# Kernel tuning notes

Measured on AMD Instinct MI355X. Metric: run time of the kernel, lower is better.

Reference implementation:

```python
import jax, jax.numpy as jnp
import numpy as np

K = 5  # kernel_size per dim, dim=2 -> 25 kernel weights, degree-1 open B-splines


def _spline_basis(pseudo):
    """Degree-1 open B-spline basis for dim=2, kernel_size=5.
    pseudo: [E,2] in [0,1]. Returns basis [E,4], kernel index wi [E,4]."""
    v = pseudo * (K - 1)                      # [E,2]
    lo = jnp.floor(v)
    frac = v - lo                             # [E,2]
    lo = lo.astype(jnp.int32)
    b = jnp.stack([1.0 - frac, frac], axis=-1)            # [E,2,2] (edge, dim, offset)
    idx = jnp.clip(lo[..., None] + jnp.arange(2, dtype=jnp.int32), 0, K - 1)  # [E,2,2]
    basis = b[:, 0, :, None] * b[:, 1, None, :]           # [E,2,2]
    wi = idx[:, 0, :, None] + K * idx[:, 1, None, :]      # [E,2,2] (dim0 stride 1, dim1 stride K)
    E = pseudo.shape[0]
    return basis.reshape(E, 4), wi.reshape(E, 4)


def _spline_conv(x, src, dst, pseudo, W, root, bias, num_nodes):
    basis, wi = _spline_basis(pseudo)          # [E,4], [E,4]
    xW = jnp.einsum('ni,kio->nko', x, W)       # [N,25,out]
    gathered = xW[src[:, None], wi]            # [E,4,out]
    msg = jnp.einsum('es,eso->eo', basis, gathered)  # [E,out]
    agg = jax.ops.segment_max(msg, dst, num_segments=num_nodes)
    agg = jnp.where(jnp.isneginf(agg), 0.0, agg)  # empty segments -> 0 (PyG fill)
    return agg + x @ root + bias


def setup_inputs() -> dict:
    key = jax.random.key(0)
    ks = jax.random.split(key, 12)
    N, E, C = 50000, 800000, 64
    s = 1.0 / np.sqrt(C)
    return {
        'x': jax.random.normal(ks[0], (N, C), jnp.float32),
        'edge_index': jax.random.randint(ks[1], (2, E), 0, N, jnp.int32),
        'edge_attr': jax.random.uniform(ks[2], (E, 2), jnp.float32),
        'W1': jax.random.normal(ks[3], (25, C, C), jnp.float32) * s,
        'root1': jax.random.normal(ks[4], (C, C), jnp.float32) * s,
        'b1': jnp.zeros((C,), jnp.float32),
        'W2': jax.random.normal(ks[5], (25, C, C), jnp.float32) * s,
        'root2': jax.random.normal(ks[6], (C, C), jnp.float32) * s,
        'b2': jnp.zeros((C,), jnp.float32),
        'final_w': jax.random.normal(ks[7], (3 * C, C), jnp.float32) / np.sqrt(3 * C),
        'final_b': jnp.zeros((C,), jnp.float32),
    }


def reference(x, edge_index, edge_attr, W1, root1, b1, W2, root2, b2, final_w, final_b):
    N = x.shape[0]
    src, dst = edge_index[0], edge_index[1]
    x1 = jax.nn.relu(_spline_conv(x, src, dst, edge_attr, W1, root1, b1, N))
    x2 = jax.nn.relu(_spline_conv(x1, src, dst, edge_attr, W2, root2, b2, N))
    h = jnp.concatenate([x, x1, x2], axis=-1)   # cat=True; dropout p=0 (eval)
    return h @ final_w + final_b
```

## Files before the change

kernel.cpp:

```cpp
#include <hip/hip_runtime.h>
#include <hip/hip_bf16.h>


typedef short  bf16x8 __attribute__((ext_vector_type(8)));
typedef float  f32x4  __attribute__((ext_vector_type(4)));

__device__ __forceinline__ float bf2f(ushort u) {
    return __uint_as_float((uint)u << 16);
}
__device__ __forceinline__ ushort f2bf(float f) {
    uint u = __float_as_uint(f);
    return (ushort)((u + 0x7FFF + ((u >> 16) & 1)) >> 16);
}

__global__ __launch_bounds__(256) void prep(
    const float* __restrict__ x, ushort* __restrict__ xb, int nx,
    const float* __restrict__ W1, const float* __restrict__ r1, ushort* __restrict__ WtA,
    const float* __restrict__ W2, const float* __restrict__ r2, ushort* __restrict__ WtB,
    const float* __restrict__ fw, ushort* __restrict__ fwT,
    int* __restrict__ deg, int N)
{
    const int nw = 26 * 4096, nfw = 3 * 4096;
    int idx = blockIdx.x * 256 + threadIdx.x;
    if (idx < nx) { xb[idx] = f2bf(x[idx]); return; }
    idx -= nx;
    if (idx < nw) {
        int tile = idx >> 12, rem = idx & 4095, o = rem >> 6, i = rem & 63;
        WtA[idx] = f2bf(tile < 25 ? W1[tile * 4096 + i * 64 + o] : r1[i * 64 + o]);
        return;
    }
    idx -= nw;
    if (idx < nw) {
        int tile = idx >> 12, rem = idx & 4095, o = rem >> 6, i = rem & 63;
        WtB[idx] = f2bf(tile < 25 ? W2[tile * 4096 + i * 64 + o] : r2[i * 64 + o]);
        return;
    }
    idx -= nw;
    if (idx < nfw) {
        int t = idx >> 12, rem = idx & 4095, o = rem >> 6, k = rem & 63;
        fwT[idx] = f2bf(fw[(t * 64 + k) * 64 + o]);
        return;
    }
    idx -= nfw;
    if (idx < N) deg[idx] = 0;
}

__global__ __launch_bounds__(256) void hist_deg(
    const int* __restrict__ ei, int* __restrict__ deg, int E)
{
    int e = blockIdx.x * 256 + threadIdx.x;
    if (e < E) atomicAdd(&deg[ei[E + e]], 1);
}

__global__ __launch_bounds__(1024) void scan_block(
    const int* __restrict__ deg, int* __restrict__ inc,
    int* __restrict__ partial, int N)
{
    __shared__ int s[1024];
    int i = blockIdx.x * 1024 + threadIdx.x;
    int v = (i < N) ? deg[i] : 0;
    s[threadIdx.x] = v;
    __syncthreads();
    for (int off = 1; off < 1024; off <<= 1) {
        int t = (threadIdx.x >= off) ? s[threadIdx.x - off] : 0;
        __syncthreads();
        s[threadIdx.x] += t;
        __syncthreads();
    }
    if (i < N) inc[i] = s[threadIdx.x];
    if (threadIdx.x == 1023) partial[blockIdx.x] = s[1023];
}

__global__ void scan_partial(int* __restrict__ partial, int nb)
{
    __shared__ int s[64];
    int t = threadIdx.x;
    int v = (t < nb) ? partial[t] : 0;
    s[t] = v;
    __syncthreads();
    for (int off = 1; off < 64; off <<= 1) {
        int x = (t >= off) ? s[t - off] : 0;
        __syncthreads();
        s[t] += x;
        __syncthreads();
    }
    if (t < nb) partial[t] = s[t] - v;
}

__global__ __launch_bounds__(1024) void scan_finalize(
    const int* __restrict__ deg, const int* __restrict__ inc,
    const int* __restrict__ partial, int* __restrict__ row_ptr,
    int* __restrict__ cursor, int N)
{
    int i = blockIdx.x * 1024 + threadIdx.x;
    if (i >= N) return;
    int v = inc[i] + partial[blockIdx.x];
    row_ptr[i + 1] = v;
    cursor[i] = v - deg[i];
    if (i == 0) row_ptr[0] = 0;
}

__global__ __launch_bounds__(256) void gemm_scatter(
    const ushort* __restrict__ A, const ushort* __restrict__ Wt,
    ushort* __restrict__ xWb, float* __restrict__ xRoot, int mtiles,
    const int* __restrict__ ei, const float* __restrict__ attr,
    int* __restrict__ cursor, int4* __restrict__ epack, int E)
{
    __shared__ ushort Cs[64][72];
    const int bx = blockIdx.x;

    if (bx >= 26) {
        if (!ei) return;
        int e = ((bx - 26) * gridDim.y + blockIdx.y) * 256 + threadIdx.x;
        if (e >= E) return;
        int src = ei[e], dst = ei[E + e];
        float u = attr[2 * e] * 4.f;
        float v = attr[2 * e + 1] * 4.f;
        float lu = floorf(u), lv = floorf(v);
        float fu = u - lu, fv = v - lv;
        int iu = (int)lu;  iu = iu < 0 ? 0 : (iu > 4 ? 4 : iu);
        int iv = (int)lv;  iv = iv < 0 ? 0 : (iv > 4 ? 4 : iv);
        int iu1 = iu + 1 > 4 ? 4 : iu + 1;
        int iv1 = iv + 1 > 4 ? 4 : iv + 1;
        uint slots = (uint)(iu + 5 * iv) | ((uint)(iu + 5 * iv1) << 8) |
                     ((uint)(iu1 + 5 * iv) << 16) | ((uint)(iu1 + 5 * iv1) << 24);
        uint wlo = (uint)f2bf((1.f - fu) * (1.f - fv)) | ((uint)f2bf((1.f - fu) * fv) << 16);
        uint whi = (uint)f2bf(fu * (1.f - fv)) | ((uint)f2bf(fu * fv) << 16);
        int pos = atomicAdd(&cursor[dst], 1);
        epack[pos] = make_int4(src * 3200, (int)slots, (int)wlo, (int)whi);
        return;
    }

    const int wave = threadIdx.x >> 6;
    const int lane = threadIdx.x & 63;
    const int l16 = lane & 15;
    const int half = lane >> 4;
    const int tid = threadIdx.x;

    const ushort* btile = Wt + (size_t)bx * 4096;
    bf16x8 b0[4], b1[4];
    #pragma unroll
    for (int s = 0; s < 4; ++s) {
        const ushort* brow = btile + (size_t)(s * 16 + l16) * 64;
        b0[s] = *(const bf16x8*)(brow + half * 8);
        b1[s] = *(const bf16x8*)(brow + 32 + half * 8);
    }

    for (int it = 0; it < 8; ++it) {
        const int mt = blockIdx.y * 8 + it;
        if (mt >= mtiles) break;
        const int m0 = mt * 64;
        const int m_base = m0 + wave * 16;

        const ushort* arow = A + (size_t)(m_base + l16) * 64;
        bf16x8 a0 = *(const bf16x8*)(arow + half * 8);
        bf16x8 a1 = *(const bf16x8*)(arow + 32 + half * 8);

        f32x4 acc[4];
        #pragma unroll
        for (int s = 0; s < 4; ++s) {
            acc[s] = (f32x4){0.f, 0.f, 0.f, 0.f};
            acc[s] = __builtin_amdgcn_mfma_f32_16x16x32_bf16(a0, b0[s], acc[s], 0, 0, 0);
            acc[s] = __builtin_amdgcn_mfma_f32_16x16x32_bf16(a1, b1[s], acc[s], 0, 0, 0);
        }

        if (bx == 25) {
            #pragma unroll
            for (int s = 0; s < 4; ++s)
                #pragma unroll
                for (int r = 0; r < 4; ++r)
                    xRoot[(size_t)(m_base + half * 4 + r) * 64 + s * 16 + l16] = acc[s][r];
            continue;
        }

        #pragma unroll
        for (int s = 0; s < 4; ++s)
            #pragma unroll
            for (int r = 0; r < 4; ++r)
                Cs[wave * 16 + half * 4 + r][s * 16 + l16] = f2bf(acc[s][r]);
        __syncthreads();
        #pragma unroll
        for (int i2 = 0; i2 < 2; ++i2) {
            int idx = tid + i2 * 256;
            int row = idx >> 3, seg = idx & 7;
            uint4 v = *(const uint4*)&Cs[row][seg * 8];
            *(uint4*)(xWb + (size_t)(m0 + row) * 1600 + bx * 64 + seg * 8) = v;
        }
        __syncthreads();
    }
}

__device__ __forceinline__ void gather4(
    const char* __restrict__ xwb, int lane, int rb, uint slots, ushort g[4])
{
    g[0] = *((const ushort*)(xwb + rb + ((slots & 255u) << 7)) + lane);
    g[1] = *((const ushort*)(xwb + rb + (((slots >> 8) & 255u) << 7)) + lane);
    g[2] = *((const ushort*)(xwb + rb + (((slots >> 16) & 255u) << 7)) + lane);
    g[3] = *((const ushort*)(xwb + rb + ((slots >> 24) << 7)) + lane);
}

__device__ __forceinline__ float consume4(const int4 d, const ushort g[4])
{
    float m = __uint_as_float((uint)d.z << 16) * bf2f(g[0]);
    m = fmaf(__uint_as_float((uint)d.z & 0xffff0000u), bf2f(g[1]), m);
    m = fmaf(__uint_as_float((uint)d.w << 16), bf2f(g[2]), m);
    m = fmaf(__uint_as_float((uint)d.w & 0xffff0000u), bf2f(g[3]), m);
    return m;
}

__global__ __launch_bounds__(256) void edge_csr(
    const ushort* __restrict__ xWb, const int* __restrict__ row_ptr,
    const int4* __restrict__ epack, const float* __restrict__ xRoot,
    const float* __restrict__ bias, float* __restrict__ outf,
    ushort* __restrict__ outb, int N)
{
    const int wv = __builtin_amdgcn_readfirstlane(threadIdx.x >> 6);
    const int d = blockIdx.x * 4 + wv;
    const int lane = threadIdx.x & 63;
    if (d >= N) return;
    const int e0 = __builtin_amdgcn_readfirstlane(row_ptr[d]);
    const int e1 = __builtin_amdgcn_readfirstlane(row_ptr[d + 1]);
    const char* xwb = (const char*)xWb;

    float vmax = -__builtin_inff();
    int e = e0;
    const int pairs = (e1 - e0) >> 1;
    if (pairs > 0) {
        int4 dA = epack[e], dB = epack[e + 1];
        ushort gA[4], gB[4];
        gather4(xwb, lane, dA.x, (uint)dA.y, gA);
        gather4(xwb, lane, dB.x, (uint)dB.y, gB);
        for (int p = 1; p < pairs; ++p) {
            int4 nA = epack[e + 2 * p], nB = epack[e + 2 * p + 1];
            ushort hA[4], hB[4];
            gather4(xwb, lane, nA.x, (uint)nA.y, hA);
            gather4(xwb, lane, nB.x, (uint)nB.y, hB);
            vmax = fmaxf(vmax, fmaxf(consume4(dA, gA), consume4(dB, gB)));
            #pragma unroll
            for (int i = 0; i < 4; ++i) { gA[i] = hA[i]; gB[i] = hB[i]; }
            dA = nA; dB = nB;
        }
        vmax = fmaxf(vmax, fmaxf(consume4(dA, gA), consume4(dB, gB)));
        e += pairs * 2;
    }
    if (e < e1) {
        int4 dA = epack[e];
        ushort gA[4];
        gather4(xwb, lane, dA.x, (uint)dA.y, gA);
        vmax = fmaxf(vmax, consume4(dA, gA));
    }
    if (e1 == e0) vmax = 0.f;
    float val = vmax + xRoot[(size_t)d * 64 + lane] + bias[lane];
    val = fmaxf(val, 0.f);
    if (outf) outf[(size_t)d * 64 + lane] = val;
    if (outb) outb[(size_t)d * 64 + lane] = f2bf(val);
}

__global__ __launch_bounds__(256) void final_mfma(
    const ushort* __restrict__ xb, const ushort* __restrict__ x1b,
    const ushort* __restrict__ x2b, const ushort* __restrict__ fwT,
    const float* __restrict__ fb, float* __restrict__ out, int M)
{
    const int wave = threadIdx.x >> 6;
    const int lane = threadIdx.x & 63;
    const int l16 = lane & 15;
    const int half = lane >> 4;
    const int m_base = blockIdx.x * 64 + wave * 16;
    const ushort* srcs[3] = {xb, x1b, x2b};

    f32x4 acc[4];
    #pragma unroll
    for (int s = 0; s < 4; ++s) acc[s] = (f32x4){0.f, 0.f, 0.f, 0.f};

    #pragma unroll
    for (int t = 0; t < 3; ++t) {
        const ushort* arow = srcs[t] + (size_t)(m_base + l16) * 64;
        bf16x8 a0 = *(const bf16x8*)(arow + half * 8);
        bf16x8 a1 = *(const bf16x8*)(arow + 32 + half * 8);
        const ushort* btile = fwT + (size_t)t * 4096;
        #pragma unroll
        for (int s = 0; s < 4; ++s) {
            const ushort* brow = btile + (size_t)(s * 16 + l16) * 64;
            bf16x8 b0 = *(const bf16x8*)(brow + half * 8);
            bf16x8 b1 = *(const bf16x8*)(brow + 32 + half * 8);
            acc[s] = __builtin_amdgcn_mfma_f32_16x16x32_bf16(a0, b0, acc[s], 0, 0, 0);
            acc[s] = __builtin_amdgcn_mfma_f32_16x16x32_bf16(a1, b1, acc[s], 0, 0, 0);
        }
    }

    #pragma unroll
    for (int s = 0; s < 4; ++s) {
        int o = s * 16 + l16;
        float b = fb[o];
        #pragma unroll
        for (int r = 0; r < 4; ++r) {
            int m = m_base + half * 4 + r;
            if (m < M) out[(size_t)m * 64 + o] = acc[s][r] + b;
        }
    }
}

extern "C" void kernel_launch(void* const* d_in, const int* in_sizes, int n_in,
                              void* d_out, int out_size, void* d_ws, size_t ws_size,
                              hipStream_t stream)
{
    const float* x    = (const float*)d_in[0];
    const int*   ei   = (const int*)d_in[1];
    const float* attr = (const float*)d_in[2];
    const float* W1   = (const float*)d_in[3];
    const float* r1   = (const float*)d_in[4];
    const float* b1   = (const float*)d_in[5];
    const float* W2   = (const float*)d_in[6];
    const float* r2   = (const float*)d_in[7];
    const float* b2   = (const float*)d_in[8];
    const float* fw   = (const float*)d_in[9];
    const float* fb   = (const float*)d_in[10];
    float* out = (float*)d_out;

    const int N = in_sizes[0] / 64;
    const int E = in_sizes[1] / 2;
    const int mtiles = (N + 63) / 64;
    const int Npad = mtiles * 64;

    char* p = (char*)d_ws;
    auto alloc = [&](size_t bytes) { void* q = p; p += (bytes + 255) & ~(size_t)255; return q; };
    int4*   epack  = (int4*)alloc((size_t)E * 16);
    float*  x1f    = (float*)alloc((size_t)Npad * 64 * 4);
    float*  xRoot  = (float*)alloc((size_t)Npad * 64 * 4);
    ushort* xWb    = (ushort*)alloc((size_t)Npad * 1600 * 2);
    ushort* xb     = (ushort*)alloc((size_t)Npad * 64 * 2);
    ushort* x1b    = (ushort*)alloc((size_t)Npad * 64 * 2);
    ushort* x2b    = (ushort*)alloc((size_t)Npad * 64 * 2);
    ushort* WtA    = (ushort*)alloc((size_t)26 * 4096 * 2);
    ushort* WtB    = (ushort*)alloc((size_t)26 * 4096 * 2);
    ushort* fwT    = (ushort*)alloc((size_t)3 * 4096 * 2);
    int*    deg    = (int*)alloc((size_t)N * 4);
    int*    cursor = (int*)alloc((size_t)N * 4);
    int*    rowp   = (int*)alloc((size_t)(N + 1) * 4);
    int*    tmpinc = (int*)alloc((size_t)N * 4);
    int*    part   = (int*)alloc(64 * 4);

    const int nb = (N + 1023) / 1024;

    const int nprep = N * 64 + 2 * 26 * 4096 + 3 * 4096 + N;
    prep<<<(nprep + 255) / 256, 256, 0, stream>>>(
        x, xb, N * 64, W1, r1, WtA, W2, r2, WtB, fw, fwT, deg, N);

    hist_deg<<<(E + 255) / 256, 256, 0, stream>>>(ei, deg, E);
    scan_block<<<nb, 1024, 0, stream>>>(deg, tmpinc, part, N);
    scan_partial<<<1, 64, 0, stream>>>(part, nb);
    scan_finalize<<<nb, 1024, 0, stream>>>(deg, tmpinc, part, rowp, cursor, N);

    const int gy = (mtiles + 7) / 8;
    const int sc_blocks = (E + 255) / 256;
    const int sc_cols = (sc_blocks + gy - 1) / gy;

    gemm_scatter<<<dim3(26 + sc_cols, gy), 256, 0, stream>>>(
        xb, WtA, xWb, xRoot, mtiles, ei, attr, cursor, epack, E);
    edge_csr<<<(N + 3) / 4, 256, 0, stream>>>(xWb, rowp, epack, xRoot, b1, x1f, x1b, N);

    gemm_scatter<<<dim3(26, gy), 256, 0, stream>>>(
        x1b, WtB, xWb, xRoot, mtiles, nullptr, nullptr, nullptr, nullptr, E);
    edge_csr<<<(N + 3) / 4, 256, 0, stream>>>(xWb, rowp, epack, xRoot, b2, nullptr, x2b, N);

    final_mfma<<<mtiles, 256, 0, stream>>>(xb, x1b, x2b, fwT, fb, out, N);
}
```

Measured before the change: 405.9 us.

## Compute all 26 weight tiles per 16-row block and store full xW rows contiguously

The per-node transform GEMM is reorganised so each block takes 16 node rows and its 4 waves loop over all 26 weight tiles, instead of one block per weight tile sweeping 8 row tiles. Results are staged in a 51KB LDS tile covering full 1600-column rows, then written to xWb as one contiguous run per block rather than 128-byte pieces spread across rows. The edge-packing scatter blocks now occupy the front of a 1D grid. The unused fp32 x1 output of the first edge pass is also dropped, removing one store stream. In exchange, B tiles are reloaded from cache for every block, and the large LDS footprint limits how many blocks fit on a CU.

```diff
diff --git a/kernel.cpp b/kernel.cpp
--- a/kernel.cpp
+++ b/kernel.cpp
@@ -100,18 +100,19 @@
     if (i == 0) row_ptr[0] = 0;
 }
 
-__global__ __launch_bounds__(256) void gemm_scatter(
+__global__ __launch_bounds__(256) void gemm16_scatter(
     const ushort* __restrict__ A, const ushort* __restrict__ Wt,
-    ushort* __restrict__ xWb, float* __restrict__ xRoot, int mtiles,
+    ushort* __restrict__ xWb, float* __restrict__ xRoot, int scb,
     const int* __restrict__ ei, const float* __restrict__ attr,
     int* __restrict__ cursor, int4* __restrict__ epack, int E)
 {
-    __shared__ ushort Cs[64][72];
+    __shared__ ushort sT[16 * 1608];
+    const int tid = threadIdx.x;
     const int bx = blockIdx.x;
 
-    if (bx >= 26) {
+    if (bx < scb) {
         if (!ei) return;
-        int e = ((bx - 26) * gridDim.y + blockIdx.y) * 256 + threadIdx.x;
+        int e = bx * 256 + tid;
         if (e >= E) return;
         int src = ei[e], dst = ei[E + e];
         float u = attr[2 * e] * 4.f;
@@ -131,62 +132,50 @@
         return;
     }
 
-    const int wave = threadIdx.x >> 6;
-    const int lane = threadIdx.x & 63;
+    const int wave = tid >> 6;
+    const int lane = tid & 63;
     const int l16 = lane & 15;
     const int half = lane >> 4;
-    const int tid = threadIdx.x;
-
-    const ushort* btile = Wt + (size_t)bx * 4096;
-    bf16x8 b0[4], b1[4];
-    #pragma unroll
-    for (int s = 0; s < 4; ++s) {
-        const ushort* brow = btile + (size_t)(s * 16 + l16) * 64;
-        b0[s] = *(const bf16x8*)(brow + half * 8);
-        b1[s] = *(const bf16x8*)(brow + 32 + half * 8);
-    }
-
-    for (int it = 0; it < 8; ++it) {
-        const int mt = blockIdx.y * 8 + it;
-        if (mt >= mtiles) break;
-        const int m0 = mt * 64;
-        const int m_base = m0 + wave * 16;
-
-        const ushort* arow = A + (size_t)(m_base + l16) * 64;
-        bf16x8 a0 = *(const bf16x8*)(arow + half * 8);
-        bf16x8 a1 = *(const bf16x8*)(arow + 32 + half * 8);
-
+    const int m0 = (bx - scb) * 16;
+
+    const ushort* arow = A + (size_t)(m0 + l16) * 64;
+    const bf16x8 a0 = *(const bf16x8*)(arow + half * 8);
+    const bf16x8 a1 = *(const bf16x8*)(arow + 32 + half * 8);
+
+    for (int t = wave; t < 26; t += 4) {
+        const ushort* btile = Wt + (size_t)t * 4096;
         f32x4 acc[4];
         #pragma unroll
         for (int s = 0; s < 4; ++s) {
+            const ushort* brow = btile + (size_t)(s * 16 + l16) * 64;
+            bf16x8 b0 = *(const bf16x8*)(brow + half * 8);
+            bf16x8 b1 = *(const bf16x8*)(brow + 32 + half * 8);
             acc[s] = (f32x4){0.f, 0.f, 0.f, 0.f};
-            acc[s] = __builtin_amdgcn_mfma_f32_16x16x32_bf16(a0, b0[s], acc[s], 0, 0, 0);
-            acc[s] = __builtin_amdgcn_mfma_f32_16x16x32_bf16(a1, b1[s], acc[s], 0, 0, 0);
-        }
-
-        if (bx == 25) {
+            acc[s] = __builtin_amdgcn_mfma_f32_16x16x32_bf16(a0, b0, acc[s], 0, 0, 0);
+            acc[s] = __builtin_amdgcn_mfma_f32_16x16x32_bf16(a1, b1, acc[s], 0, 0, 0);
+        }
+        if (t == 25) {
             #pragma unroll
             for (int s = 0; s < 4; ++s)
                 #pragma unroll
                 for (int r = 0; r < 4; ++r)
-                    xRoot[(size_t)(m_base + half * 4 + r) * 64 + s * 16 + l16] = acc[s][r];
-            continue;
-        }
-
-        #pragma unroll
-        for (int s = 0; s < 4; ++s)
+                    xRoot[(size_t)(m0 + half * 4 + r) * 64 + s * 16 + l16] = acc[s][r];
+        } else {
             #pragma unroll
-            for (int r = 0; r < 4; ++r)
-                Cs[wave * 16 + half * 4 + r][s * 16 + l16] = f2bf(acc[s][r]);
-        __syncthreads();
-        #pragma unroll
-        for (int i2 = 0; i2 < 2; ++i2) {
-            int idx = tid + i2 * 256;
-            int row = idx >> 3, seg = idx & 7;
-            uint4 v = *(const uint4*)&Cs[row][seg * 8];
-            *(uint4*)(xWb + (size_t)(m0 + row) * 1600 + bx * 64 + seg * 8) = v;
-        }
-        __syncthreads();
+            for (int s = 0; s < 4; ++s)
+                #pragma unroll
+                for (int r = 0; r < 4; ++r)
+                    sT[(half * 4 + r) * 1608 + t * 64 + s * 16 + l16] = f2bf(acc[s][r]);
+        }
+    }
+
+    __syncthreads();
+    const size_t gbase = (size_t)m0 * 1600;
+    for (int q = tid; q < 3200; q += 256) {
+        int row = q / 200;
+        int c = q - row * 200;
+        uint4 v = *(const uint4*)&sT[row * 1608 + c * 8];
+        *(uint4*)(xWb + gbase + (size_t)row * 1600 + (size_t)c * 8) = v;
     }
 }
 
@@ -325,7 +314,6 @@
     char* p = (char*)d_ws;
     auto alloc = [&](size_t bytes) { void* q = p; p += (bytes + 255) & ~(size_t)255; return q; };
     int4*   epack  = (int4*)alloc((size_t)E * 16);
-    float*  x1f    = (float*)alloc((size_t)Npad * 64 * 4);
     float*  xRoot  = (float*)alloc((size_t)Npad * 64 * 4);
     ushort* xWb    = (ushort*)alloc((size_t)Npad * 1600 * 2);
     ushort* xb     = (ushort*)alloc((size_t)Npad * 64 * 2);
@@ -351,16 +339,15 @@
     scan_partial<<<1, 64, 0, stream>>>(part, nb);
     scan_finalize<<<nb, 1024, 0, stream>>>(deg, tmpinc, part, rowp, cursor, N);
 
-    const int gy = (mtiles + 7) / 8;
+    const int nmb = mtiles * 4;
     const int sc_blocks = (E + 255) / 256;
-    const int sc_cols = (sc_blocks + gy - 1) / gy;
-
-    gemm_scatter<<<dim3(26 + sc_cols, gy), 256, 0, stream>>>(
-        xb, WtA, xWb, xRoot, mtiles, ei, attr, cursor, epack, E);
-    edge_csr<<<(N + 3) / 4, 256, 0, stream>>>(xWb, rowp, epack, xRoot, b1, x1f, x1b, N);
-
-    gemm_scatter<<<dim3(26, gy), 256, 0, stream>>>(
-        x1b, WtB, xWb, xRoot, mtiles, nullptr, nullptr, nullptr, nullptr, E);
+
+    gemm16_scatter<<<sc_blocks + nmb, 256, 0, stream>>>(
+        xb, WtA, xWb, xRoot, sc_blocks, ei, attr, cursor, epack, E);
+    edge_csr<<<(N + 3) / 4, 256, 0, stream>>>(xWb, rowp, epack, xRoot, b1, nullptr, x1b, N);
+
+    gemm16_scatter<<<nmb, 256, 0, stream>>>(
+        x1b, WtB, xWb, xRoot, 0, nullptr, nullptr, nullptr, nullptr, E);
     edge_csr<<<(N + 3) / 4, 256, 0, stream>>>(xWb, rowp, epack, xRoot, b2, nullptr, x2b, N);
 
     final_mfma<<<mtiles, 256, 0, stream>>>(xb, x1b, x2b, fwT, fb, out, N);
```

Result: slower. 514.0 us (+26.6%).
